# Optimization experiments

Measured on AMD Instinct MI355X. Metric: run time of the kernel, lower is better.

## Reference

```python
import jax, jax.numpy as jnp
import numpy as np

EPS = 0.5          # residual scaling (module __init__ eps)
N = 100_000        # num nodes
E = 1_250_000      # num edges (avg degree ~12.5)
D = 64             # feature dim


def setup_inputs() -> dict:
    key = jax.random.key(0)
    k1, k2, k3 = jax.random.split(key, 3)
    x = jax.random.normal(k1, (N, D), dtype=jnp.float32)
    src = jax.random.randint(k2, (E,), 0, N, dtype=jnp.int32)
    dst = jax.random.randint(k3, (E,), 0, N, dtype=jnp.int32)
    return {"x": x, "src": src, "dst": dst}


def reference(x, src, dst):
    n = x.shape[0]
    # out-degree of each node = number of edges with that node as source
    deg = jax.ops.segment_sum(jnp.ones(src.shape, dtype=x.dtype), src, num_segments=n)
    norm = jnp.power(jnp.maximum(deg, 1.0), -0.5)          # [N]
    edge_norm = norm[src] * norm[dst]                      # [E] (u_mul_v)
    msg = x[src] * edge_norm[:, None]                      # [E, D] (u_mul_e)
    h = jax.ops.segment_sum(msg, dst, num_segments=n)      # sum per destination
    return h + x * EPS
```

## Files before the change

kernel.cpp:

```cpp
#include <hip/hip_runtime.h>

constexpr int D        = 64;
constexpr float EPS    = 0.5f;
constexpr int BKT      = 256;
constexpr int CAPB_MAX = 4096;
constexpr int EPB      = 4096;
constexpr int PTHREADS = 512;
constexpr int EPT      = EPB / PTHREADS;
constexpr int GTHREADS = 1024;
constexpr int NTHREADS = 512;
constexpr int NBMAX    = 512;
constexpr int MAXOVF   = 65536;

__device__ __forceinline__ unsigned int f2bf(float f) {
    unsigned int u = __float_as_uint(f);
    return (u + 0x7FFFu + ((u >> 16) & 1u)) >> 16;
}
__device__ __forceinline__ float bf2f_lo(unsigned int v) { return __uint_as_float(v << 16); }
__device__ __forceinline__ float bf2f_hi(unsigned int v) { return __uint_as_float(v & 0xFFFF0000u); }


__global__ __launch_bounds__(PTHREADS)
void partition_kernel(const int* __restrict__ src, const int* __restrict__ dst,
                      int* __restrict__ curD, int* __restrict__ curS,
                      unsigned int* __restrict__ rec, unsigned char* __restrict__ srec,
                      int* __restrict__ ovf_cnt, int* __restrict__ ovf,
                      int* __restrict__ sovf_cnt, int* __restrict__ sovf,
                      int E, int NB, int capb) {
    __shared__ int histD[NBMAX];
    __shared__ int histS[NBMAX];
    __shared__ int startD[NBMAX];
    __shared__ int startS[NBMAX];
    const int base = blockIdx.x * EPB;
    const int tid  = threadIdx.x;
    const bool full = (base + EPB) <= E;
    for (int b = tid; b < NB; b += PTHREADS) { histD[b] = 0; histS[b] = 0; }
    __syncthreads();

    if (full) {
        const int4* s4 = (const int4*)(src + base);
        const int4* d4 = (const int4*)(dst + base);
        #pragma unroll
        for (int k = 0; k < EPT / 4; ++k) {
            int4 sv = s4[tid + k * PTHREADS];
            int4 dv = d4[tid + k * PTHREADS];
            atomicAdd(&histD[dv.x >> 8], 1); atomicAdd(&histS[sv.x >> 8], 1);
            atomicAdd(&histD[dv.y >> 8], 1); atomicAdd(&histS[sv.y >> 8], 1);
            atomicAdd(&histD[dv.z >> 8], 1); atomicAdd(&histS[sv.z >> 8], 1);
            atomicAdd(&histD[dv.w >> 8], 1); atomicAdd(&histS[sv.w >> 8], 1);
        }
    } else {
        for (int k = 0; k < EPT; ++k) {
            int e = base + tid + k * PTHREADS;
            if (e < E) {
                atomicAdd(&histD[dst[e] >> 8], 1);
                atomicAdd(&histS[src[e] >> 8], 1);
            }
        }
    }
    __syncthreads();
    for (int b = tid; b < NB; b += PTHREADS) {
        int c = histD[b];
        startD[b] = (c > 0) ? atomicAdd(&curD[b], c) : 0;
        histD[b] = 0;
        int c2 = histS[b];
        startS[b] = (c2 > 0) ? atomicAdd(&curS[b], c2) : 0;
        histS[b] = 0;
    }
    __syncthreads();
    if (full) {
        const int4* s4 = (const int4*)(src + base);
        const int4* d4 = (const int4*)(dst + base);
        #pragma unroll
        for (int k = 0; k < EPT / 4; ++k) {
            int4 sv = s4[tid + k * PTHREADS];
            int4 dv = d4[tid + k * PTHREADS];
            int ss[4] = {sv.x, sv.y, sv.z, sv.w};
            int tt[4] = {dv.x, dv.y, dv.z, dv.w};
            #pragma unroll
            for (int j = 0; j < 4; ++j) {
                int s = ss[j], t = tt[j];
                int bD = t >> 8;
                int r  = atomicAdd(&histD[bD], 1);
                int p  = startD[bD] + r;
                if (p < capb) {
                    rec[(size_t)bD * capb + p] = ((unsigned int)s << 8) | (unsigned int)(t & (BKT - 1));
                } else {
                    int i = atomicAdd(ovf_cnt, 1);
                    if (i < MAXOVF) { ovf[2 * i] = s; ovf[2 * i + 1] = t; }
                }
                int bS = s >> 8;
                int r2 = atomicAdd(&histS[bS], 1);
                int p2 = startS[bS] + r2;
                if (p2 < capb) {
                    srec[(size_t)bS * capb + p2] = (unsigned char)(s & (BKT - 1));
                } else {
                    int i = atomicAdd(sovf_cnt, 1);
                    if (i < MAXOVF) sovf[i] = s;
                }
            }
        }
    } else {
        for (int k = 0; k < EPT; ++k) {
            int e = base + tid + k * PTHREADS;
            if (e < E) {
                int s = src[e], t = dst[e];
                int bD = t >> 8;
                int r  = atomicAdd(&histD[bD], 1);
                int p  = startD[bD] + r;
                if (p < capb) {
                    rec[(size_t)bD * capb + p] = ((unsigned int)s << 8) | (unsigned int)(t & (BKT - 1));
                } else {
                    int i = atomicAdd(ovf_cnt, 1);
                    if (i < MAXOVF) { ovf[2 * i] = s; ovf[2 * i + 1] = t; }
                }
                int bS = s >> 8;
                int r2 = atomicAdd(&histS[bS], 1);
                int p2 = startS[bS] + r2;
                if (p2 < capb) {
                    srec[(size_t)bS * capb + p2] = (unsigned char)(s & (BKT - 1));
                } else {
                    int i = atomicAdd(sovf_cnt, 1);
                    if (i < MAXOVF) sovf[i] = s;
                }
            }
        }
    }
}

__global__ __launch_bounds__(NTHREADS)
void degnorm_kernel(const unsigned char* __restrict__ srec, const int* __restrict__ curS,
                    const int* __restrict__ sovf_cnt, const int* __restrict__ sovf,
                    float* __restrict__ norm, int n, int capb) {
    const int b   = blockIdx.x;
    const int tid = threadIdx.x;
    __shared__ int hist[BKT];
    if (tid < BKT) hist[tid] = 0;
    __syncthreads();
    int cnt = curS[b];
    if (cnt > capb) cnt = capb;
    const unsigned int* s4 = (const unsigned int*)(srec + (size_t)b * capb);
    int nw = cnt >> 2;
    for (int i = tid; i < nw; i += NTHREADS) {
        unsigned int w = s4[i];
        atomicAdd(&hist[w & 255u], 1);
        atomicAdd(&hist[(w >> 8) & 255u], 1);
        atomicAdd(&hist[(w >> 16) & 255u], 1);
        atomicAdd(&hist[w >> 24], 1);
    }
    for (int i = (nw << 2) + tid; i < cnt; i += NTHREADS)
        atomicAdd(&hist[srec[(size_t)b * capb + i]], 1);
    int oc = *sovf_cnt;
    if (oc > 0) {
        if (oc > MAXOVF) oc = MAXOVF;
        for (int i = tid; i < oc; i += NTHREADS) {
            int s = sovf[i];
            if ((s >> 8) == b) atomicAdd(&hist[s & (BKT - 1)], 1);
        }
    }
    __syncthreads();
    if (tid < BKT) {
        int node = b * BKT + tid;
        if (node < n) norm[node] = rsqrtf(fmaxf((float)hist[tid], 1.0f));
    }
}

__global__ __launch_bounds__(256)
void yhconv_kernel(const float2* __restrict__ x2, const float* __restrict__ norm,
                   unsigned int* __restrict__ yh, int total) {
    int stride = gridDim.x * 256;
    for (int i = blockIdx.x * 256 + threadIdx.x; i < total; i += stride) {
        float2 v = x2[i];
        float nm = norm[i >> 5];
        yh[i] = f2bf(v.x * nm) | (f2bf(v.y * nm) << 16);
    }
}

__global__ __launch_bounds__(GTHREADS)
void sortgather_kernel(const unsigned int* __restrict__ rec, const int* __restrict__ curD,
                       const float* __restrict__ norm, const uint4* __restrict__ yr4,
                       const float4* __restrict__ x4, float4* __restrict__ out4,
                       int n, int capb) {
    __shared__ unsigned int recs[CAPB_MAX];
    __shared__ unsigned int srcs[CAPB_MAX];
    __shared__ int hist[BKT];
    __shared__ int rankb[BKT];
    __shared__ int rsL[BKT];
    __shared__ float nrmL[BKT];
    __shared__ unsigned int wsums[GTHREADS / 64];
    const int b   = blockIdx.x;
    const int tid = threadIdx.x;
    const int lane = tid & 63;
    const int wid  = tid >> 6;

    int cnt = curD[b];
    if (cnt > capb) cnt = capb;
    for (int i = tid; i < cnt; i += GTHREADS) recs[i] = rec[(size_t)b * capb + i];
    if (tid < BKT) {
        hist[tid] = 0;
        int node = b * BKT + tid;
        nrmL[tid] = (node < n) ? norm[node] : 1.0f;
    }
    __syncthreads();
    for (int i = tid; i < cnt; i += GTHREADS) atomicAdd(&hist[recs[i] & (BKT - 1)], 1);
    __syncthreads();
    {
        int v = (tid < BKT) ? hist[tid] : 0;
        #pragma unroll
        for (int off = 1; off < 64; off <<= 1) {
            int t = __shfl_up(v, off);
            if (lane >= off) v += t;
        }
        if (tid < BKT && lane == 63) wsums[wid] = (unsigned int)v;
        __syncthreads();
        if (tid < BKT) {
            int add = 0;
            #pragma unroll
            for (int w = 0; w < BKT / 64; ++w)
                if (w < wid) add += (int)wsums[w];
            int excl = v + add - hist[tid];
            rankb[tid] = excl;
            rsL[tid]   = excl;
        }
    }
    __syncthreads();
    for (int i = tid; i < cnt; i += GTHREADS) {
        unsigned int v = recs[i];
        int pos = atomicAdd(&rankb[v & (BKT - 1)], 1);
        srcs[pos] = v >> 8;
    }
    __syncthreads();

    const int fl  = lane & 7;
    const int oct = lane >> 3;
    #pragma unroll
    for (int r = 0; r < BKT / 128; ++r) {
        int ln   = r * 128 + wid * 8 + oct;
        int node = b * BKT + ln;
        bool valid = node < n;
        int rsl = valid ? rsL[ln]  : 0;
        int cl  = valid ? hist[ln] : 0;
        int m = cl;
        m = max(m, __shfl_xor(m, 8));
        m = max(m, __shfl_xor(m, 16));
        m = max(m, __shfl_xor(m, 32));
        float a0 = 0.f, a1 = 0.f, a2 = 0.f, a3 = 0.f;
        float a4 = 0.f, a5 = 0.f, a6 = 0.f, a7 = 0.f;
        for (int k = 0; k < m; k += 8) {
            int sb[8];
            #pragma unroll
            for (int j = 0; j < 8; ++j) {
                int kj = k + j;
                sb[j] = (kj < cl) ? (int)srcs[rsl + kj] : -1;
            }
            #pragma unroll
            for (int j = 0; j < 8; ++j) {
                bool take = sb[j] >= 0;
                int s = take ? sb[j] : 0;
                uint4 v = yr4[(size_t)s * 8 + fl];
                if (!take) { v.x = 0u; v.y = 0u; v.z = 0u; v.w = 0u; }
                a0 += bf2f_lo(v.x); a1 += bf2f_hi(v.x);
                a2 += bf2f_lo(v.y); a3 += bf2f_hi(v.y);
                a4 += bf2f_lo(v.z); a5 += bf2f_hi(v.z);
                a6 += bf2f_lo(v.w); a7 += bf2f_hi(v.w);
            }
        }
        if (valid) {
            float nt = nrmL[ln];
            size_t basei = (size_t)node * 16 + fl * 2;
            float4 xv0 = x4[basei], xv1 = x4[basei + 1];
            float4 r0, r1;
            r0.x = a0 * nt + EPS * xv0.x;  r0.y = a1 * nt + EPS * xv0.y;
            r0.z = a2 * nt + EPS * xv0.z;  r0.w = a3 * nt + EPS * xv0.w;
            r1.x = a4 * nt + EPS * xv1.x;  r1.y = a5 * nt + EPS * xv1.y;
            r1.z = a6 * nt + EPS * xv1.z;  r1.w = a7 * nt + EPS * xv1.w;
            out4[basei] = r0;
            out4[basei + 1] = r1;
        }
    }
}

__global__ void cleanup_kernel(const float* __restrict__ x, const float* __restrict__ norm,
                               const int* __restrict__ ovf_cnt, const int* __restrict__ ovf,
                               float* __restrict__ out) {
    int cnt = *ovf_cnt;
    if (cnt > MAXOVF) cnt = MAXOVF;
    long long total = (long long)cnt * D;
    long long stride = (long long)gridDim.x * blockDim.x;
    for (long long i = blockIdx.x * (long long)blockDim.x + threadIdx.x; i < total; i += stride) {
        int e = (int)(i >> 6), d = (int)(i & 63);
        int s = ovf[2 * e], t = ovf[2 * e + 1];
        atomicAdd(&out[(size_t)t * D + d], norm[s] * norm[t] * x[(size_t)s * D + d]);
    }
}


__global__ void fb_hist(const int* __restrict__ src, int* __restrict__ deg, int E) {
    int e = blockIdx.x * blockDim.x + threadIdx.x;
    if (e < E) atomicAdd(&deg[src[e]], 1);
}
__global__ void fb_norm(const int* __restrict__ deg, float* __restrict__ norm, int n) {
    int i = blockIdx.x * blockDim.x + threadIdx.x;
    if (i < n) norm[i] = rsqrtf(fmaxf((float)deg[i], 1.0f));
}
__global__ void fb_init_out(const float4* __restrict__ x, float4* __restrict__ out, int n4) {
    int i = blockIdx.x * blockDim.x + threadIdx.x;
    if (i < n4) {
        float4 v = x[i];
        out[i] = make_float4(v.x * EPS, v.y * EPS, v.z * EPS, v.w * EPS);
    }
}
__global__ void fb_scatter(const float* __restrict__ x, const int* __restrict__ src,
                           const int* __restrict__ dst, const float* __restrict__ norm,
                           float* __restrict__ out, int E) {
    long long tid = (long long)blockIdx.x * blockDim.x + threadIdx.x;
    int e = (int)(tid >> 6), d = (int)(tid & 63);
    if (e < E) {
        int s = src[e], t = dst[e];
        atomicAdd(&out[(size_t)t * D + d], norm[s] * norm[t] * x[(size_t)s * D + d]);
    }
}


extern "C" void kernel_launch(void* const* d_in, const int* in_sizes, int n_in,
                              void* d_out, int out_size, void* d_ws, size_t ws_size,
                              hipStream_t stream) {
    const float* x   = (const float*)d_in[0];
    const int*   src = (const int*)d_in[1];
    const int*   dst = (const int*)d_in[2];
    float* out = (float*)d_out;

    const int ND = in_sizes[0];
    const int E  = in_sizes[1];
    const int n  = ND / D;
    const int NB = (n + BKT - 1) / BKT;
    constexpr int B = 256;
    const int NB64 = (NB + 63) & ~63;

    int capb = 0;
    for (int c : {4096, 3584}) {
        size_t srecB = ((size_t)NB * c + 15) & ~15ull;
        size_t need = (size_t)NB * c * 4
                    + srecB
                    + (size_t)ND * 2
                    + (size_t)n * 4
                    + (size_t)(2 * NB64 + 128) * 4
                    + (size_t)3 * MAXOVF * 4;
        if (need <= ws_size) { capb = c; break; }
    }

    if (NB <= NBMAX && capb > 0 && n < (1 << 24) && E > 0) {
        unsigned int* rec   = (unsigned int*)d_ws;
        unsigned char* srec = (unsigned char*)(rec + (size_t)NB * capb);
        size_t srecB        = ((size_t)NB * capb + 15) & ~15ull;
        unsigned int* yh    = (unsigned int*)(srec + srecB);
        float* norm         = (float*)(yh + ND / 2);
        int* curD           = (int*)(norm + n);
        int* curS           = curD + NB64;
        int* ovf_cnt        = curS + NB64;
        int* sovf_cnt       = ovf_cnt + 64;
        int* ovf            = sovf_cnt + 64;
        int* sovf           = ovf + 2 * MAXOVF;

        hipMemsetAsync(curD, 0, (size_t)(2 * NB64 + 128) * 4, stream);
        partition_kernel<<<(E + EPB - 1) / EPB, PTHREADS, 0, stream>>>(src, dst, curD, curS,
                                                                       rec, srec, ovf_cnt, ovf,
                                                                       sovf_cnt, sovf, E, NB, capb);
        degnorm_kernel<<<NB, NTHREADS, 0, stream>>>(srec, curS, sovf_cnt, sovf, norm, n, capb);
        int yt = ND / 2;
        int yg = (yt + 255) / 256; if (yg > 2048) yg = 2048;
        yhconv_kernel<<<yg, B, 0, stream>>>((const float2*)x, norm, yh, yt);
        sortgather_kernel<<<NB, GTHREADS, 0, stream>>>(rec, curD, norm, (const uint4*)yh,
                                                       (const float4*)x, (float4*)out, n, capb);
        cleanup_kernel<<<32, B, 0, stream>>>(x, norm, ovf_cnt, ovf, out);
    } else {
        int*   deg  = (int*)d_ws;
        float* norm = (float*)d_ws + n;
        hipMemsetAsync(deg, 0, (size_t)n * sizeof(int), stream);
        fb_hist<<<(E + B - 1) / B, B, 0, stream>>>(src, deg, E);
        fb_norm<<<(n + B - 1) / B, B, 0, stream>>>(deg, norm, n);
        fb_init_out<<<(ND / 4 + B - 1) / B, B, 0, stream>>>((const float4*)x, (float4*)out, ND / 4);
        long long total = (long long)E * D;
        fb_scatter<<<(int)((total + B - 1) / B), B, 0, stream>>>(x, src, dst, norm, out, E);
    }
}
```

Baseline: 142.7 us.

## Fuse degree-norm with bf16 prescale, sort nodes by degree, double partition chunk

Merges the degree/norm kernel with the bf16 conversion of norm-scaled x, so each bucket block writes its norms and converts its own 256 nodes' features, removing one launch and a global norm re-read. In the gather kernel, the nodes of each bucket are reordered by in-degree through an O(256) rank loop, so the 8 nodes sharing a wave have similar edge counts and the max-degree loop wastes less work. Edges per partition block are doubled, which halves the partition grid. The rank loop adds serial shared-memory work per block, and the larger partition chunk lowers parallelism.

```diff
diff --git a/kernel.cpp b/kernel.cpp
--- a/kernel.cpp
+++ b/kernel.cpp
@@ -4,7 +4,7 @@
 constexpr float EPS    = 0.5f;
 constexpr int BKT      = 256;
 constexpr int CAPB_MAX = 4096;
-constexpr int EPB      = 4096;
+constexpr int EPB      = 8192;
 constexpr int PTHREADS = 512;
 constexpr int EPT      = EPB / PTHREADS;
 constexpr int GTHREADS = 1024;
@@ -129,12 +129,14 @@
 }
 
 __global__ __launch_bounds__(NTHREADS)
-void degnorm_kernel(const unsigned char* __restrict__ srec, const int* __restrict__ curS,
-                    const int* __restrict__ sovf_cnt, const int* __restrict__ sovf,
-                    float* __restrict__ norm, int n, int capb) {
+void normyh_kernel(const unsigned char* __restrict__ srec, const int* __restrict__ curS,
+                   const int* __restrict__ sovf_cnt, const int* __restrict__ sovf,
+                   const float2* __restrict__ x2, unsigned int* __restrict__ yh,
+                   float* __restrict__ norm, int n, int capb) {
     const int b   = blockIdx.x;
     const int tid = threadIdx.x;
     __shared__ int hist[BKT];
+    __shared__ float nrm[BKT];
     if (tid < BKT) hist[tid] = 0;
     __syncthreads();
     int cnt = curS[b];
@@ -161,18 +163,20 @@
     __syncthreads();
     if (tid < BKT) {
         int node = b * BKT + tid;
-        if (node < n) norm[node] = rsqrtf(fmaxf((float)hist[tid], 1.0f));
-    }
-}
-
-__global__ __launch_bounds__(256)
-void yhconv_kernel(const float2* __restrict__ x2, const float* __restrict__ norm,
-                   unsigned int* __restrict__ yh, int total) {
-    int stride = gridDim.x * 256;
-    for (int i = blockIdx.x * 256 + threadIdx.x; i < total; i += stride) {
-        float2 v = x2[i];
-        float nm = norm[i >> 5];
-        yh[i] = f2bf(v.x * nm) | (f2bf(v.y * nm) << 16);
+        float nm = rsqrtf(fmaxf((float)hist[tid], 1.0f));
+        nrm[tid] = nm;
+        if (node < n) norm[node] = nm;
+    }
+    __syncthreads();
+    int nodes = n - b * BKT;
+    if (nodes > BKT) nodes = BKT;
+    if (nodes < 0) nodes = 0;
+    int total = nodes * (D / 2);
+    size_t gbase = (size_t)b * BKT * (D / 2);
+    for (int i = tid; i < total; i += NTHREADS) {
+        float2 v = x2[gbase + i];
+        float nm2 = nrm[i >> 5];
+        yh[gbase + i] = f2bf(v.x * nm2) | (f2bf(v.y * nm2) << 16);
     }
 }
 
@@ -186,6 +190,7 @@
     __shared__ int hist[BKT];
     __shared__ int rankb[BKT];
     __shared__ int rsL[BKT];
+    __shared__ int perm[BKT];
     __shared__ float nrmL[BKT];
     __shared__ unsigned int wsums[GTHREADS / 64];
     const int b   = blockIdx.x;
@@ -221,6 +226,13 @@
             int excl = v + add - hist[tid];
             rankb[tid] = excl;
             rsL[tid]   = excl;
+            int c = hist[tid];
+            int rk = 0;
+            for (int j = 0; j < BKT; ++j) {
+                int cj = hist[j];
+                rk += (cj < c) || ((cj == c) && (j < tid));
+            }
+            perm[rk] = tid;
         }
     }
     __syncthreads();
@@ -235,7 +247,8 @@
     const int oct = lane >> 3;
     #pragma unroll
     for (int r = 0; r < BKT / 128; ++r) {
-        int ln   = r * 128 + wid * 8 + oct;
+        int slot = r * 128 + wid * 8 + oct;
+        int ln   = perm[slot];
         int node = b * BKT + ln;
         bool valid = node < n;
         int rsl = valid ? rsL[ln]  : 0;
@@ -366,10 +379,8 @@
         partition_kernel<<<(E + EPB - 1) / EPB, PTHREADS, 0, stream>>>(src, dst, curD, curS,
                                                                        rec, srec, ovf_cnt, ovf,
                                                                        sovf_cnt, sovf, E, NB, capb);
-        degnorm_kernel<<<NB, NTHREADS, 0, stream>>>(srec, curS, sovf_cnt, sovf, norm, n, capb);
-        int yt = ND / 2;
-        int yg = (yt + 255) / 256; if (yg > 2048) yg = 2048;
-        yhconv_kernel<<<yg, B, 0, stream>>>((const float2*)x, norm, yh, yt);
+        normyh_kernel<<<NB, NTHREADS, 0, stream>>>(srec, curS, sovf_cnt, sovf,
+                                                   (const float2*)x, yh, norm, n, capb);
         sortgather_kernel<<<NB, GTHREADS, 0, stream>>>(rec, curD, norm, (const uint4*)yh,
                                                        (const float4*)x, (float4*)out, n, capb);
         cleanup_kernel<<<32, B, 0, stream>>>(x, norm, ovf_cnt, ovf, out);
```

Measured after the change: 145.4 us. Within noise of the previous version (+1.9%).
